# Kernel tuning notes

Measured on AMD Instinct MI355X. Metric: run time of the kernel, lower is better.

The kernel has to match this reference:

```python
import jax, jax.numpy as jnp
import numpy as np

N = 50000      # nodes
E = 800000     # edges (before self loops)
D = 128        # embedding_dimension
HEADS = 4
C = 32         # hidden_channels
NEG_SLOPE = 0.2


def setup_inputs() -> dict:
    key = jax.random.key(0)
    ks = jax.random.split(key, 12)
    s = 0.1
    x = jax.random.normal(ks[0], (N, D), jnp.float32)
    edge_index = jax.random.randint(ks[1], (2, E), 0, N)
    # layer 1: D -> HEADS*C, concat
    W1 = jax.random.normal(ks[2], (D, HEADS * C), jnp.float32) * s
    a_src1 = jax.random.normal(ks[3], (HEADS, C), jnp.float32) * s
    a_dst1 = jax.random.normal(ks[4], (HEADS, C), jnp.float32) * s
    b1 = jnp.zeros((HEADS * C,), jnp.float32)
    # layer 2: HEADS*C -> HEADS*C, concat
    W2 = jax.random.normal(ks[5], (HEADS * C, HEADS * C), jnp.float32) * s
    a_src2 = jax.random.normal(ks[6], (HEADS, C), jnp.float32) * s
    a_dst2 = jax.random.normal(ks[7], (HEADS, C), jnp.float32) * s
    b2 = jnp.zeros((HEADS * C,), jnp.float32)
    # layer 3: HEADS*C -> C, heads=1, no concat (mean over the single head)
    W3 = jax.random.normal(ks[8], (HEADS * C, C), jnp.float32) * s
    a_src3 = jax.random.normal(ks[9], (1, C), jnp.float32) * s
    a_dst3 = jax.random.normal(ks[10], (1, C), jnp.float32) * s
    b3 = jnp.zeros((C,), jnp.float32)
    return {"x": x, "edge_index": edge_index,
            "W1": W1, "a_src1": a_src1, "a_dst1": a_dst1, "b1": b1,
            "W2": W2, "a_src2": a_src2, "a_dst2": a_dst2, "b2": b2,
            "W3": W3, "a_src3": a_src3, "a_dst3": a_dst3, "b3": b3}


def gat_layer(x, src, dst, W, a_s, a_d, b, heads, concat):
    """One PyG-style GATConv (eval mode: dropout inactive).
    x: [N, Fin]; src/dst: [E2] (self loops included)."""
    n = x.shape[0]
    h = (x @ W).reshape(n, heads, -1)                 # [N, H, C]
    alpha_src = (h * a_s).sum(-1)                     # [N, H]
    alpha_dst = (h * a_d).sum(-1)                     # [N, H]
    logits = jax.nn.leaky_relu(alpha_src[src] + alpha_dst[dst], NEG_SLOPE)  # [E2, H]
    # segment softmax over destination nodes
    m = jax.ops.segment_max(logits, dst, num_segments=n)          # [N, H]
    ex = jnp.exp(logits - m[dst])                                  # [E2, H]
    denom = jax.ops.segment_sum(ex, dst, num_segments=n)          # [N, H]
    alpha = ex / (denom[dst] + 1e-16)                              # [E2, H]
    msg = h[src] * alpha[:, :, None]                               # [E2, H, C]
    out = jax.ops.segment_sum(msg, dst, num_segments=n)            # [N, H, C]
    if concat:
        return out.reshape(n, -1) + b
    return out.mean(axis=1) + b


def reference(x, edge_index, W1, a_src1, a_dst1, b1, W2, a_src2, a_dst2, b2,
              W3, a_src3, a_dst3, b3):
    loops = jnp.arange(N, dtype=edge_index.dtype)
    src = jnp.concatenate([edge_index[0], loops])   # add_self_loops=True
    dst = jnp.concatenate([edge_index[1], loops])
    h = gat_layer(x, src, dst, W1, a_src1, a_dst1, b1, HEADS, True)
    h = jax.nn.elu(h)
    h = gat_layer(h, src, dst, W2, a_src2, a_dst2, b2, HEADS, True)
    h = jax.nn.elu(h)
    out = gat_layer(h, src, dst, W3, a_src3, a_dst3, b3, 1, False)
    return out
```

## Files before the change

### kernel.cpp

```cpp
#include <hip/hip_runtime.h>
#include <cmath>

constexpr int NN  = 50000;
constexpr int EE  = 800000;
constexpr int E2C = EE + NN;

constexpr int NBUCK = 256;
constexpr int BW    = 196;
constexpr int EPT   = 8;
constexpr int CH    = 256 * EPT;
constexpr int NB_B  = (E2C + CH - 1) / CH;
constexpr int CAP   = 4096;
constexpr int SCAP  = 5120;
constexpr int G1ALL = (NN + 63) / 64;
constexpr int G1A   = 391;

constexpr float RLN2 = 1.44269504088896340736f;

using bf16x8 = __attribute__((ext_vector_type(8))) short;
using f32x4  = __attribute__((ext_vector_type(4))) float;

__device__ inline unsigned bf16rne(float f) {
    unsigned u = __builtin_bit_cast(unsigned, f);
    return (u + 0x7fffu + ((u >> 16) & 1u)) >> 16;
}
__device__ inline float bflo(unsigned u) { return __builtin_bit_cast(float, u << 16); }
__device__ inline float bfhi(unsigned u) { return __builtin_bit_cast(float, u & 0xffff0000u); }

__global__ __launch_bounds__(256) void cvt_weights(
    const float* __restrict__ W1, const float* __restrict__ W2,
    const float* __restrict__ W3,
    unsigned short* __restrict__ W1t, unsigned short* __restrict__ W2t,
    unsigned short* __restrict__ W3t, int* __restrict__ bcursor,
    float* __restrict__ AS1, float* __restrict__ AS2, float* __restrict__ AS3,
    unsigned short* __restrict__ H1, unsigned short* __restrict__ H2,
    unsigned short* __restrict__ H3)
{
    int g = blockIdx.x * 256 + threadIdx.x;
    if (g < NBUCK) bcursor[g] = 0;
    if (g < 4) { AS1[NN * 4 + g] = -1e30f; AS2[NN * 4 + g] = -1e30f; }
    if (g == 4) AS3[NN] = -1e30f;
    if (g < 128) { H1[(size_t)NN * 128 + g] = 0; H2[(size_t)NN * 128 + g] = 0; }
    if (g < 32)  H3[(size_t)NN * 32 + g] = 0;

    const float* W; unsigned short* Wt; int cols;
    if (g < 2048)      { W = W1; Wt = W1t; cols = 128; }
    else if (g < 4096) { W = W2; Wt = W2t; cols = 128; g -= 2048; }
    else if (g < 4608) { W = W3; Wt = W3t; cols = 32;  g -= 4096; }
    else return;
    int c  = g / 16;
    int k8 = (g % 16) * 8;
    unsigned up[4];
    #pragma unroll
    for (int j = 0; j < 4; ++j) {
        float a = W[(k8 + 2 * j) * cols + c];
        float b = W[(k8 + 2 * j + 1) * cols + c];
        up[j] = bf16rne(a) | (bf16rne(b) << 16);
    }
    uint4 u; u.x = up[0]; u.y = up[1]; u.z = up[2]; u.w = up[3];
    *(uint4*)(Wt + c * 128 + k8) = u;
}

template<int NT, int NH, bool F32IN>
__device__ inline void gemm_body(
    int bid, const void* __restrict__ inv, const unsigned short* __restrict__ Wt,
    const float* __restrict__ a_s, const float* __restrict__ a_d,
    unsigned short* __restrict__ hout, float* __restrict__ asrc,
    float* __restrict__ adst)
{
    constexpr int COLS = NT * 16;
    constexpr int TPH  = NT / NH;
    const int lane = threadIdx.x & 63;
    const int wave = threadIdx.x >> 6;
    const int m    = lane & 15;
    const int quad = lane >> 4;
    const int n0   = bid * 64 + wave * 16;

    int arow = n0 + m; if (arow >= NN) arow = NN - 1;

    f32x4 acc[NT] = {};
    #pragma unroll
    for (int kq = 0; kq < 4; ++kq) {
        bf16x8 a;
        if constexpr (F32IN) {
            const float* ap = (const float*)inv + (long long)arow * 128 + quad * 8 + kq * 32;
            float4 v0 = *(const float4*)ap;
            float4 v1 = *(const float4*)(ap + 4);
            a[0] = (short)bf16rne(v0.x); a[1] = (short)bf16rne(v0.y);
            a[2] = (short)bf16rne(v0.z); a[3] = (short)bf16rne(v0.w);
            a[4] = (short)bf16rne(v1.x); a[5] = (short)bf16rne(v1.y);
            a[6] = (short)bf16rne(v1.z); a[7] = (short)bf16rne(v1.w);
        } else {
            a = *(const bf16x8*)((const unsigned short*)inv
                    + (long long)arow * 128 + quad * 8 + kq * 32);
        }
        #pragma unroll
        for (int t = 0; t < NT; ++t) {
            bf16x8 b = *(const bf16x8*)(Wt + (t * 16 + m) * 128 + kq * 32 + quad * 8);
            acc[t] = __builtin_amdgcn_mfma_f32_16x16x32_bf16(a, b, acc[t], 0, 0, 0);
        }
    }

    #pragma unroll
    for (int r = 0; r < 4; ++r) {
        int node = n0 + quad * 4 + r;
        if (node < NN) {
            #pragma unroll
            for (int t = 0; t < NT; ++t)
                hout[(long long)node * COLS + t * 16 + m] =
                    (unsigned short)bf16rne(acc[t][r]);
        }
    }

    float asv[NT], adv[NT];
    #pragma unroll
    for (int t = 0; t < NT; ++t) {
        asv[t] = a_s[t * 16 + m] * RLN2;
        adv[t] = a_d[t * 16 + m] * RLN2;
    }

    #pragma unroll
    for (int r = 0; r < 4; ++r) {
        const int node = n0 + quad * 4 + r;
        #pragma unroll
        for (int hh = 0; hh < NH; ++hh) {
            float ps = 0.f, pd = 0.f;
            #pragma unroll
            for (int q = 0; q < TPH; ++q) {
                int t = hh * TPH + q;
                ps = fmaf(acc[t][r], asv[t], ps);
                pd = fmaf(acc[t][r], adv[t], pd);
            }
            #pragma unroll
            for (int off = 8; off > 0; off >>= 1) {
                ps += __shfl_down(ps, off, 16);
                pd += __shfl_down(pd, off, 16);
            }
            if (m == 0 && node < NN) {
                asrc[node * NH + hh] = ps;
                adst[node * NH + hh] = pd;
            }
        }
    }
}

__device__ inline void bin_body(
    int bid, const int* __restrict__ ei, int* __restrict__ bcursor,
    unsigned* __restrict__ pairs)
{
    __shared__ int cnt[NBUCK];
    __shared__ int scanex[NBUCK];
    __shared__ int base[NBUCK];
    __shared__ int cur[NBUCK];
    __shared__ unsigned stage[CH];

    const int tid = threadIdx.x;
    const long long e0 = (long long)bid * CH;
    cnt[tid] = 0;
    __syncthreads();

    unsigned rec[EPT]; int bk[EPT];
    #pragma unroll
    for (int j = 0; j < EPT; ++j) {
        long long e = e0 + tid + j * 256;
        bool valid = e < E2C;
        int ss = 0, dd = 0;
        if (valid) {
            if (e < EE) { ss = ei[e]; dd = ei[EE + e]; }
            else        { ss = dd = (int)(e - EE); }
        }
        int b = dd / BW;
        bk[j]  = valid ? b : -1;
        rec[j] = (unsigned)ss | ((unsigned)(dd - b * BW) << 16) | ((unsigned)b << 24);
        if (valid) atomicAdd(&cnt[b], 1);
    }
    __syncthreads();

    const int myc = cnt[tid];
    scanex[tid] = myc;
    __syncthreads();
    for (int off = 1; off < NBUCK; off <<= 1) {
        int t = (tid >= off) ? scanex[tid - off] : 0;
        __syncthreads();
        scanex[tid] += t;
        __syncthreads();
    }
    int excl = scanex[tid] - myc;
    __syncthreads();
    scanex[tid] = excl;
    cur[tid]    = excl;
    base[tid]   = atomicAdd(&bcursor[tid], myc);
    __syncthreads();

    #pragma unroll
    for (int j = 0; j < EPT; ++j) {
        if (bk[j] >= 0) {
            int p = atomicAdd(&cur[bk[j]], 1);
            stage[p] = rec[j];
        }
    }
    __syncthreads();

    const int total = (e0 + CH <= E2C) ? CH : (int)(E2C - e0);
    for (int j = tid; j < total; j += 256) {
        unsigned p = stage[j];
        int b = (int)(p >> 24);
        pairs[(size_t)b * CAP + base[b] + (j - scanex[b])] = p;
    }
}

__device__ inline void sort_body(
    int b, const int* __restrict__ bcursor, const unsigned* __restrict__ pairs,
    int2* __restrict__ rowp, unsigned short* __restrict__ sorted_src,
    unsigned short* __restrict__ perm)
{
    __shared__ int deg[256];
    __shared__ int scn[256];
    __shared__ int cur[256];
    __shared__ int hist2[64];
    __shared__ int scn2[64];
    __shared__ int cur2[64];
    const int n0 = b * BW;
    const int n1 = (n0 + BW < NN) ? n0 + BW : NN;
    const int nloc = n1 - n0;
    const int tid = threadIdx.x;
    const int mycnt = bcursor[b];
    const unsigned* seg = pairs + (size_t)b * CAP;
    const int base = b * SCAP;

    deg[tid] = 0;
    if (tid < 64) hist2[tid] = 0;
    __syncthreads();
    for (int i = tid; i < mycnt; i += 256)
        atomicAdd(&deg[(seg[i] >> 16) & 0xff], 1);
    __syncthreads();

    const int pv = (deg[tid] + 3) & ~3;
    int it = pv >> 2; if (it > 63) it = 63;
    it = 63 - it;
    scn[tid] = pv;
    if (tid < nloc) atomicAdd(&hist2[it], 1);
    __syncthreads();
    for (int off = 1; off < 256; off <<= 1) {
        int t = (tid >= off) ? scn[tid - off] : 0;
        __syncthreads();
        scn[tid] += t;
        __syncthreads();
    }
    if (tid < 64) scn2[tid] = hist2[tid];
    __syncthreads();
    for (int off = 1; off < 64; off <<= 1) {
        int t = (tid >= off && tid < 64) ? scn2[tid - off] : 0;
        __syncthreads();
        if (tid < 64) scn2[tid] += t;
        __syncthreads();
    }
    if (tid < 64) cur2[tid] = scn2[tid] - hist2[tid];
    __syncthreads();

    const int totalp = scn[255];
    const int pexcl  = scn[tid] - pv;
    cur[tid] = base + pexcl;
    if (tid < nloc) {
        int rank = atomicAdd(&cur2[it], 1);
        perm[n0 + rank] = (unsigned short)(n0 + tid);
        rowp[n0 + rank] = make_int2(base + pexcl, base + pexcl + pv);
    }
    __syncthreads();

    int lim = totalp + 8; if (lim > SCAP) lim = SCAP;
    for (int i = tid; i < lim; i += 256)
        sorted_src[base + i] = (unsigned short)NN;
    if (b == NBUCK - 1 && tid < 8)
        sorted_src[NBUCK * SCAP + tid] = (unsigned short)NN;
    __syncthreads();
    for (int i = tid; i < mycnt; i += 256) {
        unsigned p = seg[i];
        int pos = atomicAdd(&cur[(p >> 16) & 0xff], 1);
        sorted_src[pos] = (unsigned short)(p & 0xffff);
    }
}

__global__ __launch_bounds__(256) void bin_gemm(
    const int* __restrict__ ei, int* __restrict__ bcursor,
    unsigned* __restrict__ pairs,
    const float* __restrict__ x, const unsigned short* __restrict__ Wt,
    const float* __restrict__ a_s, const float* __restrict__ a_d,
    unsigned short* __restrict__ hout, float* __restrict__ asrc,
    float* __restrict__ adst)
{
    if (blockIdx.x < NB_B)
        bin_body(blockIdx.x, ei, bcursor, pairs);
    else
        gemm_body<8, 4, true>(blockIdx.x - NB_B, x, Wt, a_s, a_d, hout, asrc, adst);
}

__global__ __launch_bounds__(256) void sort_gemm(
    const int* __restrict__ bcursor, const unsigned* __restrict__ pairs,
    int2* __restrict__ rowp, unsigned short* __restrict__ sorted_src,
    unsigned short* __restrict__ perm,
    const float* __restrict__ x, const unsigned short* __restrict__ Wt,
    const float* __restrict__ a_s, const float* __restrict__ a_d,
    unsigned short* __restrict__ hout, float* __restrict__ asrc,
    float* __restrict__ adst)
{
    if (blockIdx.x < NBUCK)
        sort_body(blockIdx.x, bcursor, pairs, rowp, sorted_src, perm);
    else
        gemm_body<8, 4, true>(blockIdx.x - NBUCK + G1A, x, Wt, a_s, a_d,
                              hout, asrc, adst);
}

template<int COLS, int NH>
__device__ inline void aggr_range(
    int b0, int e0, int head, float ad,
    const unsigned short* __restrict__ sorted_src,
    const uint* __restrict__ hp,
    const float* __restrict__ asrc,
    float num[8], float& den)
{
    constexpr int USTR = COLS / 2;
    ushort4 sv = *(const ushort4*)&sorted_src[b0];
    for (int i = b0; i < e0; i += 4) {
        ushort4 nx = *(const ushort4*)&sorted_src[i + 4];
        const int s[4] = {sv.x, sv.y, sv.z, sv.w};
        float a[4];
        uint4 Hv[4];
        #pragma unroll
        for (int j = 0; j < 4; ++j) a[j] = asrc[s[j] * NH + head];
        #pragma unroll
        for (int j = 0; j < 4; ++j)
            Hv[j] = *(const uint4*)&hp[(long long)s[j] * USTR];
        #pragma unroll
        for (int j = 0; j < 4; ++j) {
            float l = a[j] + ad; l = l > 0.f ? l : 0.2f * l;
            float w;
            asm("v_exp_f32 %0, %1" : "=v"(w) : "v"(l));
            den += w;
            num[0] = fmaf(w, bflo(Hv[j].x), num[0]); num[1] = fmaf(w, bfhi(Hv[j].x), num[1]);
            num[2] = fmaf(w, bflo(Hv[j].y), num[2]); num[3] = fmaf(w, bfhi(Hv[j].y), num[3]);
            num[4] = fmaf(w, bflo(Hv[j].z), num[4]); num[5] = fmaf(w, bfhi(Hv[j].z), num[5]);
            num[6] = fmaf(w, bflo(Hv[j].w), num[6]); num[7] = fmaf(w, bfhi(Hv[j].w), num[7]);
        }
        sv = nx;
    }
}

template<int NT_OUT, int NH_OUT>
__global__ __launch_bounds__(512) void aggr_gemm(
    const unsigned short* __restrict__ perm,
    const int2* __restrict__ rowp, const unsigned short* __restrict__ sorted_src,
    const unsigned short* __restrict__ hin,
    const float* __restrict__ asrc_in, const float* __restrict__ adst_in,
    const float* __restrict__ bias,
    const unsigned short* __restrict__ Wt,
    const float* __restrict__ a_s, const float* __restrict__ a_d,
    unsigned short* __restrict__ hout, float* __restrict__ asrc_out,
    float* __restrict__ adst_out)
{
    __shared__ unsigned short lds_h[16 * 128];
    __shared__ int lds_node[16];
    __shared__ float lds_p[256][9];
    const int tid   = threadIdx.x;
    const int split = tid >> 8;
    const int t8    = tid & 255;
    const int row   = t8 >> 4;
    const int lc    = t8 & 15;
    const int rk    = blockIdx.x * 16 + row;
    const int d     = perm[rk];
    if (split == 0 && lc == 0) lds_node[row] = d;

    const int cc   = lc * 8;
    const int head = cc / 32;
    const float ad = adst_in[d * 4 + head];
    const uint* hp = (const uint*)hin + cc / 2;

    const int2 be = rowp[rk];
    const int beg = be.x, end = be.y;
    const int half = (end - beg) >> 1;
    const int mid  = beg + ((half + 3) & ~3);
    const int b0 = split ? mid : beg;
    const int e0 = split ? end : mid;

    float num[8] = {};
    float den = 0.f;
    aggr_range<128, 4>(b0, e0, head, ad, sorted_src, hp, asrc_in, num, den);

    if (split) {
        #pragma unroll
        for (int j = 0; j < 8; ++j) lds_p[t8][j] = num[j];
        lds_p[t8][8] = den;
    }
    __syncthreads();

    if (!split) {
        #pragma unroll
        for (int j = 0; j < 8; ++j) num[j] += lds_p[t8][j];
        den += lds_p[t8][8];
        float inv = 1.f / (den + 1e-16f);
        float v[8];
        #pragma unroll
        for (int j = 0; j < 8; ++j) {
            v[j] = num[j] * inv + bias[cc + j];
            v[j] = v[j] > 0.f ? v[j] : expm1f(v[j]);
        }
        uint4 u;
        u.x = bf16rne(v[0]) | (bf16rne(v[1]) << 16);
        u.y = bf16rne(v[2]) | (bf16rne(v[3]) << 16);
        u.z = bf16rne(v[4]) | (bf16rne(v[5]) << 16);
        u.w = bf16rne(v[6]) | (bf16rne(v[7]) << 16);
        *(uint4*)((char*)lds_h + row * 256 + ((lc * 16) ^ ((row & 7) << 4))) = u;
    }
    __syncthreads();
    if (split) return;

    const int lane = t8 & 63;
    const int wave = t8 >> 6;
    const int m    = lane & 15;
    const int quad = lane >> 4;
    int t0;
    if constexpr (NT_OUT == 8) t0 = wave * 2;
    else { if (wave != 0) return; t0 = 0; }

    f32x4 acc[2] = {};
    #pragma unroll
    for (int kq = 0; kq < 4; ++kq) {
        int colb = (quad * 16 + kq * 64) ^ ((m & 7) << 4);
        bf16x8 a = *(const bf16x8*)((const char*)lds_h + m * 256 + colb);
        #pragma unroll
        for (int tt = 0; tt < 2; ++tt) {
            bf16x8 b = *(const bf16x8*)(Wt + ((t0 + tt) * 16 + m) * 128
                                        + kq * 32 + quad * 8);
            acc[tt] = __builtin_amdgcn_mfma_f32_16x16x32_bf16(a, b, acc[tt], 0, 0, 0);
        }
    }

    constexpr int COLS_OUT = NT_OUT * 16;
    const int headw = t0 / (NT_OUT / NH_OUT);
    float asv[2], adv[2];
    #pragma unroll
    for (int tt = 0; tt < 2; ++tt) {
        asv[tt] = a_s[(t0 + tt) * 16 + m] * RLN2;
        adv[tt] = a_d[(t0 + tt) * 16 + m] * RLN2;
    }

    #pragma unroll
    for (int r = 0; r < 4; ++r) {
        const int node = lds_node[quad * 4 + r];
        #pragma unroll
        for (int tt = 0; tt < 2; ++tt)
            hout[(long long)node * COLS_OUT + (t0 + tt) * 16 + m] =
                (unsigned short)bf16rne(acc[tt][r]);
        float ps = acc[0][r] * asv[0];
        ps = fmaf(acc[1][r], asv[1], ps);
        float pd = acc[0][r] * adv[0];
        pd = fmaf(acc[1][r], adv[1], pd);
        #pragma unroll
        for (int off = 8; off > 0; off >>= 1) {
            ps += __shfl_down(ps, off, 16);
            pd += __shfl_down(pd, off, 16);
        }
        if (m == 0) {
            asrc_out[node * NH_OUT + headw] = ps;
            adst_out[node * NH_OUT + headw] = pd;
        }
    }
}

template<int COLS, int NH>
__global__ __launch_bounds__(256) void aggr_final(
    const unsigned short* __restrict__ perm,
    const int2* __restrict__ rowp, const unsigned short* __restrict__ sorted_src,
    const unsigned short* __restrict__ hin,
    const float* __restrict__ asrc, const float* __restrict__ adst,
    const float* __restrict__ bias, float* __restrict__ out)
{
    constexpr int TPN = COLS / 8;
    int t = blockIdx.x * 256 + threadIdx.x;
    int rk = t / TPN;
    int lc = t % TPN;
    if (rk >= NN) return;
    const int d = perm[rk];
    const int cc = lc * 8;
    const int head = cc / 32;
    const float ad = adst[d * NH + head];
    const int2 be = rowp[rk];
    const uint* hp = (const uint*)hin + cc / 2;
    float num[8] = {};
    float den = 0.f;
    aggr_range<COLS, NH>(be.x, be.y, head, ad, sorted_src, hp, asrc, num, den);
    float inv = 1.f / (den + 1e-16f);
    float v[8];
    #pragma unroll
    for (int j = 0; j < 8; ++j) v[j] = num[j] * inv + bias[cc + j];
    float4 o0 = {v[0], v[1], v[2], v[3]};
    float4 o1 = {v[4], v[5], v[6], v[7]};
    *(float4*)&out[(long long)d * COLS + lc * 8]     = o0;
    *(float4*)&out[(long long)d * COLS + lc * 8 + 4] = o1;
}

extern "C" void kernel_launch(void* const* d_in, const int* in_sizes, int n_in,
                              void* d_out, int out_size, void* d_ws, size_t ws_size,
                              hipStream_t stream)
{
    const float* x   = (const float*)d_in[0];
    const int*   ei  = (const int*)  d_in[1];
    const float* W1  = (const float*)d_in[2];
    const float* as1 = (const float*)d_in[3];
    const float* ad1 = (const float*)d_in[4];
    const float* b1  = (const float*)d_in[5];
    const float* W2  = (const float*)d_in[6];
    const float* as2 = (const float*)d_in[7];
    const float* ad2 = (const float*)d_in[8];
    const float* b2  = (const float*)d_in[9];
    const float* W3  = (const float*)d_in[10];
    const float* as3 = (const float*)d_in[11];
    const float* ad3 = (const float*)d_in[12];
    const float* b3  = (const float*)d_in[13];
    float* out = (float*)d_out;

    unsigned short* H1  = (unsigned short*)d_ws;
    unsigned short* H2  = H1 + (size_t)(NN + 1) * 128;
    unsigned short* H3  = H2 + (size_t)(NN + 1) * 128;
    unsigned short* W1t = H3 + (size_t)(NN + 1) * 32;
    unsigned short* W2t = W1t + 128 * 128;
    unsigned short* W3t = W2t + 128 * 128;
    float* AS1 = (float*)(W3t + 32 * 128);
    float* AD1 = AS1 + (size_t)(NN + 1) * 4;
    float* AS2 = AD1 + (size_t)NN * 4;
    float* AD2 = AS2 + (size_t)(NN + 1) * 4;
    float* AS3 = AD2 + (size_t)NN * 4;
    float* AD3 = AS3 + (size_t)(NN + 1);
    int2* rowp = (int2*)(AD3 + NN);
    unsigned short* sorted = (unsigned short*)(rowp + NN);
    int* bcursor = (int*)(sorted + (size_t)NBUCK * SCAP + 8);
    unsigned short* perm = (unsigned short*)(bcursor + NBUCK);
    size_t off = ((size_t)(perm + NN) - (size_t)d_ws + 15) & ~(size_t)15;
    unsigned* pairs = (unsigned*)((char*)d_ws + off);

    const int gCvtW  = (4608 + 255) / 256;
    const int gBinG  = NB_B + G1A;
    const int gSortG = NBUCK + (G1ALL - G1A);
    const int gFused = NN / 16;
    const int gAggr3 = (NN * 4 + 255) / 256;

    cvt_weights<<<gCvtW, 256, 0, stream>>>(W1, W2, W3, W1t, W2t, W3t, bcursor,
                                           AS1, AS2, AS3, H1, H2, H3);
    bin_gemm<<<gBinG, 256, 0, stream>>>(ei, bcursor, pairs,
                                        x, W1t, as1, ad1, H1, AS1, AD1);
    sort_gemm<<<gSortG, 256, 0, stream>>>(bcursor, pairs, rowp, sorted, perm,
                                          x, W1t, as1, ad1, H1, AS1, AD1);
    aggr_gemm<8, 4><<<gFused, 512, 0, stream>>>(
        perm, rowp, sorted, H1, AS1, AD1, b1, W2t, as2, ad2, H2, AS2, AD2);
    aggr_gemm<2, 1><<<gFused, 512, 0, stream>>>(
        perm, rowp, sorted, H2, AS2, AD2, b2, W3t, as3, ad3, H3, AS3, AD3);
    aggr_final<32, 1><<<gAggr3, 256, 0, stream>>>(
        perm, rowp, sorted, H3, AS3, AD3, b3, out);
}
```

Before: 253.5 us.

## Bin edges by source chunk and dst bucket with global atomics; drop split aggregation

Edge binning now writes each edge directly into one of 16×256 (source-chunk, dst-bucket) segments using a global atomic cursor. This replaces the per-block LDS histogram, scan and staging. The sort pass walks the 16 chunk segments in order, so the sorted source lists gain source locality, which should help the gathers in later layers. The fused aggregate+GEMM kernels drop the 512-thread two-way split of each node's edge range and run 256 threads, with one thread group covering all edges of a row. This removes an LDS reduction and some barriers but lowers per-node parallelism, and it adds global atomic contention plus a fixed segment capacity of 512 entries.

```diff
diff --git a/kernel.cpp b/kernel.cpp
--- a/kernel.cpp
+++ b/kernel.cpp
@@ -7,10 +7,13 @@
 
 constexpr int NBUCK = 256;
 constexpr int BW    = 196;
+constexpr int NCH   = 16;
+constexpr int CW    = 3125;
+constexpr int NSEG  = NCH * NBUCK;
+constexpr int SCAP2 = 512;
 constexpr int EPT   = 8;
 constexpr int CH    = 256 * EPT;
 constexpr int NB_B  = (E2C + CH - 1) / CH;
-constexpr int CAP   = 4096;
 constexpr int SCAP  = 5120;
 constexpr int G1ALL = (NN + 63) / 64;
 constexpr int G1A   = 391;
@@ -37,7 +40,7 @@
     unsigned short* __restrict__ H3)
 {
     int g = blockIdx.x * 256 + threadIdx.x;
-    if (g < NBUCK) bcursor[g] = 0;
+    if (g < NSEG) bcursor[g] = 0;
     if (g < 4) { AS1[NN * 4 + g] = -1e30f; AS2[NN * 4 + g] = -1e30f; }
     if (g == 4) AS3[NN] = -1e30f;
     if (g < 128) { H1[(size_t)NN * 128 + g] = 0; H2[(size_t)NN * 128 + g] = 0; }
@@ -148,64 +151,22 @@
     int bid, const int* __restrict__ ei, int* __restrict__ bcursor,
     unsigned* __restrict__ pairs)
 {
-    __shared__ int cnt[NBUCK];
-    __shared__ int scanex[NBUCK];
-    __shared__ int base[NBUCK];
-    __shared__ int cur[NBUCK];
-    __shared__ unsigned stage[CH];
-
     const int tid = threadIdx.x;
     const long long e0 = (long long)bid * CH;
-    cnt[tid] = 0;
-    __syncthreads();
-
-    unsigned rec[EPT]; int bk[EPT];
     #pragma unroll
     for (int j = 0; j < EPT; ++j) {
         long long e = e0 + tid + j * 256;
-        bool valid = e < E2C;
-        int ss = 0, dd = 0;
-        if (valid) {
+        if (e < E2C) {
+            int ss, dd;
             if (e < EE) { ss = ei[e]; dd = ei[EE + e]; }
             else        { ss = dd = (int)(e - EE); }
-        }
-        int b = dd / BW;
-        bk[j]  = valid ? b : -1;
-        rec[j] = (unsigned)ss | ((unsigned)(dd - b * BW) << 16) | ((unsigned)b << 24);
-        if (valid) atomicAdd(&cnt[b], 1);
-    }
-    __syncthreads();
-
-    const int myc = cnt[tid];
-    scanex[tid] = myc;
-    __syncthreads();
-    for (int off = 1; off < NBUCK; off <<= 1) {
-        int t = (tid >= off) ? scanex[tid - off] : 0;
-        __syncthreads();
-        scanex[tid] += t;
-        __syncthreads();
-    }
-    int excl = scanex[tid] - myc;
-    __syncthreads();
-    scanex[tid] = excl;
-    cur[tid]    = excl;
-    base[tid]   = atomicAdd(&bcursor[tid], myc);
-    __syncthreads();
-
-    #pragma unroll
-    for (int j = 0; j < EPT; ++j) {
-        if (bk[j] >= 0) {
-            int p = atomicAdd(&cur[bk[j]], 1);
-            stage[p] = rec[j];
-        }
-    }
-    __syncthreads();
-
-    const int total = (e0 + CH <= E2C) ? CH : (int)(E2C - e0);
-    for (int j = tid; j < total; j += 256) {
-        unsigned p = stage[j];
-        int b = (int)(p >> 24);
-        pairs[(size_t)b * CAP + base[b] + (j - scanex[b])] = p;
+            int c = ss / CW;
+            int b = dd / BW;
+            int seg = c * NBUCK + b;
+            int p = atomicAdd(&bcursor[seg], 1);
+            pairs[(size_t)seg * SCAP2 + p] =
+                (unsigned)ss | ((unsigned)(dd - b * BW) << 16);
+        }
     }
 }
 
@@ -224,15 +185,17 @@
     const int n1 = (n0 + BW < NN) ? n0 + BW : NN;
     const int nloc = n1 - n0;
     const int tid = threadIdx.x;
-    const int mycnt = bcursor[b];
-    const unsigned* seg = pairs + (size_t)b * CAP;
     const int base = b * SCAP;
 
     deg[tid] = 0;
     if (tid < 64) hist2[tid] = 0;
     __syncthreads();
-    for (int i = tid; i < mycnt; i += 256)
-        atomicAdd(&deg[(seg[i] >> 16) & 0xff], 1);
+    for (int c = 0; c < NCH; ++c) {
+        const unsigned* seg = pairs + (size_t)(c * NBUCK + b) * SCAP2;
+        const int n_c = bcursor[c * NBUCK + b];
+        for (int i = tid; i < n_c; i += 256)
+            atomicAdd(&deg[(seg[i] >> 16) & 0xff], 1);
+    }
     __syncthreads();
 
     const int pv = (deg[tid] + 3) & ~3;
@@ -274,10 +237,16 @@
     if (b == NBUCK - 1 && tid < 8)
         sorted_src[NBUCK * SCAP + tid] = (unsigned short)NN;
     __syncthreads();
-    for (int i = tid; i < mycnt; i += 256) {
-        unsigned p = seg[i];
-        int pos = atomicAdd(&cur[(p >> 16) & 0xff], 1);
-        sorted_src[pos] = (unsigned short)(p & 0xffff);
+
+    for (int c = 0; c < NCH; ++c) {
+        const unsigned* seg = pairs + (size_t)(c * NBUCK + b) * SCAP2;
+        const int n_c = bcursor[c * NBUCK + b];
+        for (int i = tid; i < n_c; i += 256) {
+            unsigned p = seg[i];
+            int pos = atomicAdd(&cur[(p >> 16) & 0xff], 1);
+            sorted_src[pos] = (unsigned short)(p & 0xffff);
+        }
+        __syncthreads();
     }
 }
 
@@ -347,7 +316,7 @@
 }
 
 template<int NT_OUT, int NH_OUT>
-__global__ __launch_bounds__(512) void aggr_gemm(
+__global__ __launch_bounds__(256) void aggr_gemm(
     const unsigned short* __restrict__ perm,
     const int2* __restrict__ rowp, const unsigned short* __restrict__ sorted_src,
     const unsigned short* __restrict__ hin,
@@ -360,62 +329,40 @@
 {
     __shared__ unsigned short lds_h[16 * 128];
     __shared__ int lds_node[16];
-    __shared__ float lds_p[256][9];
-    const int tid   = threadIdx.x;
-    const int split = tid >> 8;
-    const int t8    = tid & 255;
-    const int row   = t8 >> 4;
-    const int lc    = t8 & 15;
-    const int rk    = blockIdx.x * 16 + row;
-    const int d     = perm[rk];
-    if (split == 0 && lc == 0) lds_node[row] = d;
+    const int tid = threadIdx.x;
+    const int row = tid >> 4;
+    const int lc  = tid & 15;
+    const int rk  = blockIdx.x * 16 + row;
+    const int d   = perm[rk];
+    if (lc == 0) lds_node[row] = d;
 
     const int cc   = lc * 8;
     const int head = cc / 32;
     const float ad = adst_in[d * 4 + head];
     const uint* hp = (const uint*)hin + cc / 2;
-
     const int2 be = rowp[rk];
-    const int beg = be.x, end = be.y;
-    const int half = (end - beg) >> 1;
-    const int mid  = beg + ((half + 3) & ~3);
-    const int b0 = split ? mid : beg;
-    const int e0 = split ? end : mid;
 
     float num[8] = {};
     float den = 0.f;
-    aggr_range<128, 4>(b0, e0, head, ad, sorted_src, hp, asrc_in, num, den);
-
-    if (split) {
-        #pragma unroll
-        for (int j = 0; j < 8; ++j) lds_p[t8][j] = num[j];
-        lds_p[t8][8] = den;
-    }
-    __syncthreads();
-
-    if (!split) {
-        #pragma unroll
-        for (int j = 0; j < 8; ++j) num[j] += lds_p[t8][j];
-        den += lds_p[t8][8];
-        float inv = 1.f / (den + 1e-16f);
-        float v[8];
-        #pragma unroll
-        for (int j = 0; j < 8; ++j) {
-            v[j] = num[j] * inv + bias[cc + j];
-            v[j] = v[j] > 0.f ? v[j] : expm1f(v[j]);
-        }
-        uint4 u;
-        u.x = bf16rne(v[0]) | (bf16rne(v[1]) << 16);
-        u.y = bf16rne(v[2]) | (bf16rne(v[3]) << 16);
-        u.z = bf16rne(v[4]) | (bf16rne(v[5]) << 16);
-        u.w = bf16rne(v[6]) | (bf16rne(v[7]) << 16);
-        *(uint4*)((char*)lds_h + row * 256 + ((lc * 16) ^ ((row & 7) << 4))) = u;
-    }
-    __syncthreads();
-    if (split) return;
-
-    const int lane = t8 & 63;
-    const int wave = t8 >> 6;
+    aggr_range<128, 4>(be.x, be.y, head, ad, sorted_src, hp, asrc_in, num, den);
+
+    float inv = 1.f / (den + 1e-16f);
+    float v[8];
+    #pragma unroll
+    for (int j = 0; j < 8; ++j) {
+        v[j] = num[j] * inv + bias[cc + j];
+        v[j] = v[j] > 0.f ? v[j] : expm1f(v[j]);
+    }
+    uint4 u;
+    u.x = bf16rne(v[0]) | (bf16rne(v[1]) << 16);
+    u.y = bf16rne(v[2]) | (bf16rne(v[3]) << 16);
+    u.z = bf16rne(v[4]) | (bf16rne(v[5]) << 16);
+    u.w = bf16rne(v[6]) | (bf16rne(v[7]) << 16);
+    *(uint4*)((char*)lds_h + row * 256 + ((lc * 16) ^ ((row & 7) << 4))) = u;
+    __syncthreads();
+
+    const int lane = tid & 63;
+    const int wave = tid >> 6;
     const int m    = lane & 15;
     const int quad = lane >> 4;
     int t0;
@@ -534,7 +481,7 @@
     int2* rowp = (int2*)(AD3 + NN);
     unsigned short* sorted = (unsigned short*)(rowp + NN);
     int* bcursor = (int*)(sorted + (size_t)NBUCK * SCAP + 8);
-    unsigned short* perm = (unsigned short*)(bcursor + NBUCK);
+    unsigned short* perm = (unsigned short*)(bcursor + NSEG);
     size_t off = ((size_t)(perm + NN) - (size_t)d_ws + 15) & ~(size_t)15;
     unsigned* pairs = (unsigned*)((char*)d_ws + off);
 
@@ -550,9 +497,9 @@
                                         x, W1t, as1, ad1, H1, AS1, AD1);
     sort_gemm<<<gSortG, 256, 0, stream>>>(bcursor, pairs, rowp, sorted, perm,
                                           x, W1t, as1, ad1, H1, AS1, AD1);
-    aggr_gemm<8, 4><<<gFused, 512, 0, stream>>>(
+    aggr_gemm<8, 4><<<gFused, 256, 0, stream>>>(
         perm, rowp, sorted, H1, AS1, AD1, b1, W2t, as2, ad2, H2, AS2, AD2);
-    aggr_gemm<2, 1><<<gFused, 512, 0, stream>>>(
+    aggr_gemm<2, 1><<<gFused, 256, 0, stream>>>(
         perm, rowp, sorted, H2, AS2, AD2, b2, W3t, as3, ad3, H3, AS3, AD3);
     aggr_final<32, 1><<<gAggr3, 256, 0, stream>>>(
         perm, rowp, sorted, H3, AS3, AD3, b3, out);
```

Result: slower. 314.8 us (+24.2%).

## Sort edges by source within buckets and drop split aggregation in aggr_gemm

Applied to the files above, without the earlier changes.

The bucket sort scatter now runs in 16 passes over source-id ranges, so each destination's edge list comes out roughly ordered by source node. This should improve locality of the gathered source features in later aggregation. The aggr_gemm kernels also stop splitting each edge list across two thread halves with an LDS reduction and use 256 threads per block instead. That trades intra-row parallelism for lower sync and LDS overhead, while the sort pays 16 rescans of its segment.

```diff
diff --git a/kernel.cpp b/kernel.cpp
--- a/kernel.cpp
+++ b/kernel.cpp
@@ -7,6 +7,8 @@
 
 constexpr int NBUCK = 256;
 constexpr int BW    = 196;
+constexpr int NCH   = 16;
+constexpr int CW    = 3125;
 constexpr int EPT   = 8;
 constexpr int CH    = 256 * EPT;
 constexpr int NB_B  = (E2C + CH - 1) / CH;
@@ -274,10 +276,18 @@
     if (b == NBUCK - 1 && tid < 8)
         sorted_src[NBUCK * SCAP + tid] = (unsigned short)NN;
     __syncthreads();
-    for (int i = tid; i < mycnt; i += 256) {
-        unsigned p = seg[i];
-        int pos = atomicAdd(&cur[(p >> 16) & 0xff], 1);
-        sorted_src[pos] = (unsigned short)(p & 0xffff);
+
+    for (int c = 0; c < NCH; ++c) {
+        const unsigned lo = (unsigned)(c * CW), hi = lo + CW;
+        for (int i = tid; i < mycnt; i += 256) {
+            unsigned p = seg[i];
+            unsigned ss = p & 0xffffu;
+            if (ss >= lo && ss < hi) {
+                int pos = atomicAdd(&cur[(p >> 16) & 0xff], 1);
+                sorted_src[pos] = (unsigned short)ss;
+            }
+        }
+        __syncthreads();
     }
 }
 
@@ -347,7 +357,7 @@
 }
 
 template<int NT_OUT, int NH_OUT>
-__global__ __launch_bounds__(512) void aggr_gemm(
+__global__ __launch_bounds__(256) void aggr_gemm(
     const unsigned short* __restrict__ perm,
     const int2* __restrict__ rowp, const unsigned short* __restrict__ sorted_src,
     const unsigned short* __restrict__ hin,
@@ -360,62 +370,40 @@
 {
     __shared__ unsigned short lds_h[16 * 128];
     __shared__ int lds_node[16];
-    __shared__ float lds_p[256][9];
-    const int tid   = threadIdx.x;
-    const int split = tid >> 8;
-    const int t8    = tid & 255;
-    const int row   = t8 >> 4;
-    const int lc    = t8 & 15;
-    const int rk    = blockIdx.x * 16 + row;
-    const int d     = perm[rk];
-    if (split == 0 && lc == 0) lds_node[row] = d;
+    const int tid = threadIdx.x;
+    const int row = tid >> 4;
+    const int lc  = tid & 15;
+    const int rk  = blockIdx.x * 16 + row;
+    const int d   = perm[rk];
+    if (lc == 0) lds_node[row] = d;
 
     const int cc   = lc * 8;
     const int head = cc / 32;
     const float ad = adst_in[d * 4 + head];
     const uint* hp = (const uint*)hin + cc / 2;
-
     const int2 be = rowp[rk];
-    const int beg = be.x, end = be.y;
-    const int half = (end - beg) >> 1;
-    const int mid  = beg + ((half + 3) & ~3);
-    const int b0 = split ? mid : beg;
-    const int e0 = split ? end : mid;
 
     float num[8] = {};
     float den = 0.f;
-    aggr_range<128, 4>(b0, e0, head, ad, sorted_src, hp, asrc_in, num, den);
-
-    if (split) {
-        #pragma unroll
-        for (int j = 0; j < 8; ++j) lds_p[t8][j] = num[j];
-        lds_p[t8][8] = den;
-    }
-    __syncthreads();
-
-    if (!split) {
-        #pragma unroll
-        for (int j = 0; j < 8; ++j) num[j] += lds_p[t8][j];
-        den += lds_p[t8][8];
-        float inv = 1.f / (den + 1e-16f);
-        float v[8];
-        #pragma unroll
-        for (int j = 0; j < 8; ++j) {
-            v[j] = num[j] * inv + bias[cc + j];
-            v[j] = v[j] > 0.f ? v[j] : expm1f(v[j]);
-        }
-        uint4 u;
-        u.x = bf16rne(v[0]) | (bf16rne(v[1]) << 16);
-        u.y = bf16rne(v[2]) | (bf16rne(v[3]) << 16);
-        u.z = bf16rne(v[4]) | (bf16rne(v[5]) << 16);
-        u.w = bf16rne(v[6]) | (bf16rne(v[7]) << 16);
-        *(uint4*)((char*)lds_h + row * 256 + ((lc * 16) ^ ((row & 7) << 4))) = u;
-    }
-    __syncthreads();
-    if (split) return;
-
-    const int lane = t8 & 63;
-    const int wave = t8 >> 6;
+    aggr_range<128, 4>(be.x, be.y, head, ad, sorted_src, hp, asrc_in, num, den);
+
+    float inv = 1.f / (den + 1e-16f);
+    float v[8];
+    #pragma unroll
+    for (int j = 0; j < 8; ++j) {
+        v[j] = num[j] * inv + bias[cc + j];
+        v[j] = v[j] > 0.f ? v[j] : expm1f(v[j]);
+    }
+    uint4 u;
+    u.x = bf16rne(v[0]) | (bf16rne(v[1]) << 16);
+    u.y = bf16rne(v[2]) | (bf16rne(v[3]) << 16);
+    u.z = bf16rne(v[4]) | (bf16rne(v[5]) << 16);
+    u.w = bf16rne(v[6]) | (bf16rne(v[7]) << 16);
+    *(uint4*)((char*)lds_h + row * 256 + ((lc * 16) ^ ((row & 7) << 4))) = u;
+    __syncthreads();
+
+    const int lane = tid & 63;
+    const int wave = tid >> 6;
     const int m    = lane & 15;
     const int quad = lane >> 4;
     int t0;
@@ -550,9 +538,9 @@
                                         x, W1t, as1, ad1, H1, AS1, AD1);
     sort_gemm<<<gSortG, 256, 0, stream>>>(bcursor, pairs, rowp, sorted, perm,
                                           x, W1t, as1, ad1, H1, AS1, AD1);
-    aggr_gemm<8, 4><<<gFused, 512, 0, stream>>>(
+    aggr_gemm<8, 4><<<gFused, 256, 0, stream>>>(
         perm, rowp, sorted, H1, AS1, AD1, b1, W2t, as2, ad2, H2, AS2, AD2);
-    aggr_gemm<2, 1><<<gFused, 512, 0, stream>>>(
+    aggr_gemm<2, 1><<<gFused, 256, 0, stream>>>(
         perm, rowp, sorted, H2, AS2, AD2, b2, W3t, as3, ad3, H3, AS3, AD3);
     aggr_final<32, 1><<<gAggr3, 256, 0, stream>>>(
         perm, rowp, sorted, H3, AS3, AD3, b3, out);
```

Result: slower. 284.6 us (+12.3%).
